# Kernel optimization log

Measured on AMD Instinct MI355X. Metric: run time of the kernel, lower is better.

Reference implementation:

```python
import jax, jax.numpy as jnp
import numpy as np

B, S, D, H, DH = 2, 4096, 768, 12, 64
BS, NB, L, FF, VOCAB = 16, 256, 2, 3072, 50358
SCALE = 1.0 / np.sqrt(DH)


def _ln(x, g, b, eps=1e-12):
    m = jnp.mean(x, -1, keepdims=True)
    v = jnp.var(x, -1, keepdims=True)
    return (x - m) * jax.lax.rsqrt(v + eps) * g + b


def _make_key_block_idx(seed=0):
    rng = np.random.default_rng(seed)
    idx = np.zeros((NB, 7), np.int32)
    allb = np.arange(NB)
    for i in range(NB):
        req = sorted({0, NB - 1, max(i - 1, 0), i, min(i + 1, NB - 1)})
        pool = np.setdiff1d(allb, req)
        extra = rng.choice(pool, size=7 - len(req), replace=False)
        idx[i] = np.concatenate([req, extra])
    return jnp.asarray(idx)


def _sparse_attn(q, k, v, key_idx):
    # q,k,v: [B,H,NB,BS,DH]; key_idx: [NB,7]
    kg = k[:, :, key_idx].reshape(B, H, NB, 7 * BS, DH)  # gather key blocks
    vg = v[:, :, key_idx].reshape(B, H, NB, 7 * BS, DH)
    s = jnp.einsum('bhnqd,bhnkd->bhnqk', q, kg) * SCALE
    o = jnp.einsum('bhnqk,bhnkd->bhnqd', jax.nn.softmax(s, -1), vg)
    # first/last query blocks: full (global) attention over all keys
    qe = q[:, :, jnp.array([0, NB - 1])]                 # [B,H,2,BS,DH]
    kf = k.reshape(B, H, S, DH)
    vf = v.reshape(B, H, S, DH)
    se = jnp.einsum('bhgqd,bhkd->bhgqk', qe, kf) * SCALE
    oe = jnp.einsum('bhgqk,bhkd->bhgqd', jax.nn.softmax(se, -1), vf)
    o = o.at[:, :, 0].set(oe[:, :, 0]).at[:, :, NB - 1].set(oe[:, :, 1])
    # [B,H,NB,BS,DH] -> [B,S,D]
    return o.transpose(0, 2, 3, 1, 4).reshape(B, S, D)


def setup_inputs():
    key = jax.random.key(0)
    ks = iter(jax.random.split(key, 24))
    n = lambda sh, s=0.02: jax.random.normal(next(ks), sh, jnp.float32) * s
    inp = {
        'input_ids': jax.random.randint(next(ks), (B, S), 0, VOCAB),
        'key_block_idx': _make_key_block_idx(),
        'embed': n((VOCAB, D)),
        'Wqkv': n((L, D, 3 * D)), 'bqkv': jnp.zeros((L, 3 * D)),
        'Wo': n((L, D, D)), 'bo': jnp.zeros((L, D)),
        'ln1_g': jnp.ones((L, D)), 'ln1_b': jnp.zeros((L, D)),
        'Wff1': n((L, D, FF)), 'bff1': jnp.zeros((L, FF)),
        'Wff2': n((L, FF, D)), 'bff2': jnp.zeros((L, D)),
        'ln2_g': jnp.ones((L, D)), 'ln2_b': jnp.zeros((L, D)),
        'Wp': n((D, D)), 'bp': jnp.zeros((D,)),
        'start_w': jax.random.normal(next(ks), (D,)),
        'end_w': jax.random.normal(next(ks), (D,)),
        'd1_W': n((D, 20)), 'd1_b': jnp.zeros((20,)),
        'd2_W': n((20, 2)), 'd2_b': jnp.zeros((2,)),
    }
    return inp


def reference(input_ids, key_block_idx, embed, Wqkv, bqkv, Wo, bo, ln1_g, ln1_b,
              Wff1, bff1, Wff2, bff2, ln2_g, ln2_b, Wp, bp, start_w, end_w,
              d1_W, d1_b, d2_W, d2_b):
    x = embed[input_ids]                                  # [B,S,D]
    for l in range(L):
        qkv = x @ Wqkv[l] + bqkv[l]
        q, k, v = jnp.split(qkv, 3, axis=-1)
        blk = lambda t: t.reshape(B, NB, BS, H, DH).transpose(0, 3, 1, 2, 4)
        a = _sparse_attn(blk(q), blk(k), blk(v), key_block_idx)
        x = _ln(x + a @ Wo[l] + bo[l], ln1_g[l], ln1_b[l])
        h = jax.nn.gelu(x @ Wff1[l] + bff1[l]) @ Wff2[l] + bff2[l]
        x = _ln(x + h, ln2_g[l], ln2_b[l])
    pool = jnp.tanh(x[:, 0] @ Wp + bp)                    # BigBird pooler
    start_probs = jax.nn.softmax(x @ start_w, -1)         # [B,S]
    end_probs = jax.nn.softmax(x @ end_w, -1)
    d = (pool[0] @ d1_W + d1_b) @ d2_W + d2_b             # no ReLU, as in source
    disc = jax.nn.softmax(d, -1)
    return start_probs, end_probs, disc
```

## Files before the change

kernel.cpp:

```cpp
#include <hip/hip_runtime.h>
#include <hip/hip_bf16.h>
#include <math.h>

#define B_   2
#define S_   4096
#define D_   768
#define H_   12
#define DH_  64
#define BS_  16
#define NB_  256
#define FF_  3072
#define BT_  (B_ * S_)
#define SCALE_F 0.125f

#define NSPLIT 32
#define TILES_PER_SPLIT (NB_ / NSPLIT)
#define NEDGE (B_ * H_ * 2)
#define NSPARSE (B_ * H_ * NB_)
#define NXCD 8

typedef _Float16 f16x8 __attribute__((ext_vector_type(8)));
typedef _Float16 f16x4 __attribute__((ext_vector_type(4)));
typedef _Float16 f16x2 __attribute__((ext_vector_type(2)));
typedef float    f32x4 __attribute__((ext_vector_type(4)));
typedef float    f32x16 __attribute__((ext_vector_type(16)));

#define DKS 8
#define DKC (D_ / DKS)

#define SV2(v, k) __builtin_shufflevector(v, v, k, (k) + 1)

__device__ __forceinline__ int xcd_swz(int bid, int nwg)
{
    int q = nwg / NXCD;
    return (bid % NXCD) * q + bid / NXCD;
}

__device__ __forceinline__ float dot2acc(f16x2 a, f16x2 b, float c)
{
#if __has_builtin(__builtin_amdgcn_fdot2)
    return __builtin_amdgcn_fdot2(a, b, c, false);
#else
    return c + (float)a[0] * (float)b[0] + (float)a[1] * (float)b[1];
#endif
}

#define GLD16(gp, lp) __builtin_amdgcn_global_load_lds( \
    (const __attribute__((address_space(1))) void*)(gp), \
    (__attribute__((address_space(3))) void*)(lp), 16, 0, 0)

__device__ __forceinline__ float fast_tanh(float z)
{
    float az = fabsf(z);
    float t = __expf(-2.0f * az);
    float r = (1.0f - t) / (1.0f + t);
    return z < 0.f ? -r : r;
}

__device__ __forceinline__ float gelu_tanh(float v)
{
    float v3 = v * v * v;
    return 0.5f * v * (1.0f + fast_tanh(0.79788456080286535588f * (v + 0.044715f * v3)));
}

struct WSeg { const float* src; _Float16* dst; int K; int N; int start; };
struct WSegs { WSeg s[8]; int total; };

__global__ __launch_bounds__(256) void prep_all(
    WSegs segs, const int* __restrict__ ids, const float* __restrict__ emb,
    _Float16* __restrict__ xh)
{
    int bt = blockIdx.x;
    int t = threadIdx.x;
    if (bt < segs.total) {
        __shared__ float tile[32][33];
        int si = 0;
#pragma unroll
        for (int u = 1; u < 8; ++u)
            if (bt >= segs.s[u].start) si = u;
        const WSeg& sg = segs.s[si];
        int tid = bt - sg.start;
        int tn = sg.N >> 5;
        int n0 = (tid % tn) * 32;
        int k0 = (tid / tn) * 32;

        {
            int r = t >> 3, c = (t & 7) * 4;
            f32x4 v = *(const f32x4*)&sg.src[(size_t)(k0 + r) * sg.N + n0 + c];
            tile[r][c + 0] = v[0];
            tile[r][c + 1] = v[1];
            tile[r][c + 2] = v[2];
            tile[r][c + 3] = v[3];
        }
        __syncthreads();
        {
            int r = t >> 3, c = (t & 7) * 4;
            f16x4 o;
            o[0] = (_Float16)tile[c + 0][r];
            o[1] = (_Float16)tile[c + 1][r];
            o[2] = (_Float16)tile[c + 2][r];
            o[3] = (_Float16)tile[c + 3][r];
            *(f16x4*)&sg.dst[(size_t)(n0 + r) * sg.K + k0 + c] = o;
        }
    } else {
        int row = bt - segs.total;
        int id = ids[row];
        const float* src = emb + (size_t)id * D_;
        _Float16* dst16 = xh + (size_t)row * D_;
        for (int d = t; d < D_; d += 256)
            dst16[d] = (_Float16)src[d];
    }
}

template<int MI, int DBUF, int ACT, int OUT16>
__global__ __launch_bounds__(256) void gemm_f16(
    const _Float16* __restrict__ A, const _Float16* __restrict__ Wt,
    const float* __restrict__ bias, void* __restrict__ Cp,
    int M, int N, int K, int NT128)
{
    constexpr int BM = MI * 64;
    constexpr int QA = 2 * MI;
    constexpr int ASZ = BM * 64;
    constexpr int BSZ = 128 * 64;

    __shared__ __attribute__((aligned(16))) _Float16 As[(DBUF ? 2 : 1) * ASZ];
    __shared__ __attribute__((aligned(16))) _Float16 Bs[(DBUF ? 2 : 1) * BSZ];

    int t = threadIdx.x;
    int w = t >> 6, l = t & 63;
    int swz = xcd_swz(blockIdx.x, gridDim.x);
    int bm = (swz / NT128) * BM, bn = (swz % NT128) * 128;
    int wr = (w >> 1) * (MI * 32), wc = (w & 1) * 64;

    f32x16 acc[MI][2];
#pragma unroll
    for (int i = 0; i < MI; ++i)
#pragma unroll
        for (int j = 0; j < 2; ++j)
#pragma unroll
            for (int r = 0; r < 16; ++r) acc[i][j][r] = 0.f;

    const _Float16* gA[QA];
    const _Float16* gB[4];
#pragma unroll
    for (int q = 0; q < QA; ++q) {
        int m = w * QA + q;
        int row = m * 8 + (l >> 3);
        int sc = (l & 7) ^ (row & 7);
        gA[q] = A + (size_t)(bm + row) * K + sc * 8;
    }
#pragma unroll
    for (int q = 0; q < 4; ++q) {
        int m = w * 4 + q;
        int row = m * 8 + (l >> 3);
        int sc = (l & 7) ^ (row & 7);
        gB[q] = Wt + (size_t)(bn + row) * K + sc * 8;
    }

    int aoff[4][MI], boff[4][2];
#pragma unroll
    for (int kk = 0; kk < 4; ++kk) {
        int ch = (kk * 2 + (l >> 5)) ^ (l & 7);
#pragma unroll
        for (int i = 0; i < MI; ++i)
            aoff[kk][i] = (wr + i * 32 + (l & 31)) * 64 + ch * 8;
#pragma unroll
        for (int j = 0; j < 2; ++j)
            boff[kk][j] = (wc + j * 32 + (l & 31)) * 64 + ch * 8;
    }

#define STAGE_(BUF, K0)                                                   \
    {                                                                     \
        _Float16* ab_ = As + (BUF) * ASZ;                                 \
        _Float16* bb_ = Bs + (BUF) * BSZ;                                 \
        _Pragma("unroll")                                                 \
        for (int q = 0; q < QA; ++q)                                      \
            GLD16(gA[q] + (K0), ab_ + (w * QA + q) * 512);                \
        _Pragma("unroll")                                                 \
        for (int q = 0; q < 4; ++q)                                       \
            GLD16(gB[q] + (K0), bb_ + (w * 4 + q) * 512);                 \
    }

#define COMPUTE_(BUF)                                                     \
    {                                                                     \
        const _Float16* ab_ = As + (BUF) * ASZ;                           \
        const _Float16* bb_ = Bs + (BUF) * BSZ;                           \
        _Pragma("unroll")                                                 \
        for (int kk = 0; kk < 4; ++kk) {                                  \
            f16x8 af[MI], bf[2];                                          \
            _Pragma("unroll")                                             \
            for (int i = 0; i < MI; ++i)                                  \
                af[i] = *(const f16x8*)(ab_ + aoff[kk][i]);               \
            _Pragma("unroll")                                             \
            for (int j = 0; j < 2; ++j)                                   \
                bf[j] = *(const f16x8*)(bb_ + boff[kk][j]);               \
            _Pragma("unroll")                                             \
            for (int i = 0; i < MI; ++i)                                  \
                _Pragma("unroll")                                         \
                for (int j = 0; j < 2; ++j)                               \
                    acc[i][j] = __builtin_amdgcn_mfma_f32_32x32x16_f16(   \
                        af[i], bf[j], acc[i][j], 0, 0, 0);                \
        }                                                                 \
    }

    if (DBUF) {
        STAGE_(0, 0);
        __syncthreads();
        int cur = 0;
#pragma unroll 2
        for (int k0 = 0; k0 < K; k0 += 64) {
            if (k0 + 64 < K) STAGE_(cur ^ 1, k0 + 64);
            COMPUTE_(cur);
            __syncthreads();
            cur ^= 1;
        }
    } else {
        for (int k0 = 0; k0 < K; k0 += 64) {
            STAGE_(0, k0);
            __syncthreads();
            COMPUTE_(0);
            __syncthreads();
        }
    }
#undef STAGE_
#undef COMPUTE_

#pragma unroll
    for (int i = 0; i < MI; ++i) {
#pragma unroll
        for (int j = 0; j < 2; ++j) {
            int col = bn + wc + j * 32 + (l & 31);
            float bv = bias[col];
#pragma unroll
            for (int rg = 0; rg < 4; ++rg) {
                int row0 = bm + wr + i * 32 + 8 * rg + 4 * (l >> 5);
#pragma unroll
                for (int r = 0; r < 4; ++r) {
                    float v = acc[i][j][rg * 4 + r] + bv;
                    if (ACT) v = gelu_tanh(v);
                    if (OUT16)
                        ((_Float16*)Cp)[(size_t)(row0 + r) * N + col] = (_Float16)v;
                    else
                        ((float*)Cp)[(size_t)(row0 + r) * N + col] = v;
                }
            }
        }
    }
}

template<int NT, bool EDGE>
__device__ __forceinline__ void attn_block(
    const _Float16* __restrict__ qkv, const int* __restrict__ key_idx,
    _Float16* __restrict__ outp, float* __restrict__ pm,
    float* __restrict__ pl, float* __restrict__ pacc,
    int b, int h, int n, int split, int be,
    _Float16 (*qs)[72], _Float16 (*ks)[16][72],
    _Float16 (*vpl)[8][64][2], _Float16 (*ps16)[24])
{
    int t = threadIdx.x;
    int i = t >> 4;
    int c = t & 15;
    int c4 = c * 4;

    *(f16x4*)&qs[i][c4] =
        *(const f16x4*)&qkv[((size_t)(b * S_ + n * BS_ + i)) * (3 * D_) + h * DH_ + c4];
    int kb0 = EDGE ? split * NT : key_idx[n * 7];
    const _Float16* kp0 = qkv + ((size_t)(b * S_ + kb0 * BS_ + i)) * (3 * D_) + D_ + h * DH_;
    f16x4 kr = *(const f16x4*)(kp0 + c4);
    f16x4 vr = *(const f16x4*)(kp0 + D_ + c4);
    __syncthreads();

    f16x8 qv[8];
#pragma unroll
    for (int d0 = 0; d0 < 8; ++d0) qv[d0] = *(const f16x8*)&qs[i][d0 * 8];

    *(f16x4*)&ks[0][i][c4] = kr;
#pragma unroll
    for (int u = 0; u < 4; ++u) vpl[0][i >> 1][c4 + u][i & 1] = vr[u];
    if (NT > 1) {
        int kb1 = EDGE ? (split * NT + 1) : key_idx[n * 7 + 1];
        const _Float16* kp1 = qkv + ((size_t)(b * S_ + kb1 * BS_ + i)) * (3 * D_) + D_ + h * DH_;
        kr = *(const f16x4*)(kp1 + c4);
        vr = *(const f16x4*)(kp1 + D_ + c4);
    }
    __syncthreads();

    float m_old = -1e30f, lsum = 0.f;
    float acc0 = 0.f, acc1 = 0.f, acc2 = 0.f, acc3 = 0.f;
    const f16x2 one2 = {(_Float16)1.f, (_Float16)1.f};

#pragma unroll 1
    for (int jj = 0; jj < NT; ++jj) {
        int cur = jj & 1;
        if (jj + 1 < NT) {
            *(f16x4*)&ks[cur ^ 1][i][c4] = kr;
#pragma unroll
            for (int u = 0; u < 4; ++u) vpl[cur ^ 1][i >> 1][c4 + u][i & 1] = vr[u];
        }
        if (jj + 2 < NT) {
            int kb2 = EDGE ? (split * NT + jj + 2) : key_idx[n * 7 + jj + 2];
            const _Float16* kp2 = qkv + ((size_t)(b * S_ + kb2 * BS_ + i)) * (3 * D_) + D_ + h * DH_;
            kr = *(const f16x4*)(kp2 + c4);
            vr = *(const f16x4*)(kp2 + D_ + c4);
        }

        __builtin_amdgcn_s_setprio(1);
        float s0 = 0.f, s1 = 0.f;
#pragma unroll
        for (int d0 = 0; d0 < 8; ++d0) {
            f16x8 kv = *(const f16x8*)&ks[cur][c][d0 * 8];
            s0 = dot2acc(SV2(qv[d0], 0), SV2(kv, 0), s0);
            s1 = dot2acc(SV2(qv[d0], 2), SV2(kv, 2), s1);
            s0 = dot2acc(SV2(qv[d0], 4), SV2(kv, 4), s0);
            s1 = dot2acc(SV2(qv[d0], 6), SV2(kv, 6), s1);
        }
        float s = (s0 + s1) * SCALE_F;

        float rm = s;
#pragma unroll
        for (int off = 8; off; off >>= 1) rm = fmaxf(rm, __shfl_xor(rm, off, 64));
        float m_new = fmaxf(m_old, rm);
        float p = __expf(s - m_new);

        ps16[i][c] = (_Float16)p;
        f16x8 plo = *(const f16x8*)&ps16[i][0];
        f16x8 phi = *(const f16x8*)&ps16[i][8];

        float rs = 0.f;
        rs = dot2acc(SV2(plo, 0), one2, rs);
        rs = dot2acc(SV2(plo, 2), one2, rs);
        rs = dot2acc(SV2(plo, 4), one2, rs);
        rs = dot2acc(SV2(plo, 6), one2, rs);
        rs = dot2acc(SV2(phi, 0), one2, rs);
        rs = dot2acc(SV2(phi, 2), one2, rs);
        rs = dot2acc(SV2(phi, 4), one2, rs);
        rs = dot2acc(SV2(phi, 6), one2, rs);

        float corr = __expf(m_old - m_new);
        lsum = lsum * corr + rs;
        acc0 *= corr; acc1 *= corr; acc2 *= corr; acc3 *= corr;

#define PVJ(JP, PSRC, OFF)                                            \
        {                                                             \
            f16x8 vv = *(const f16x8*)&vpl[cur][JP][c4][0];           \
            f16x2 pp = SV2(PSRC, OFF);                                \
            acc0 = dot2acc(pp, SV2(vv, 0), acc0);                     \
            acc1 = dot2acc(pp, SV2(vv, 2), acc1);                     \
            acc2 = dot2acc(pp, SV2(vv, 4), acc2);                     \
            acc3 = dot2acc(pp, SV2(vv, 6), acc3);                     \
        }
        PVJ(0, plo, 0) PVJ(1, plo, 2) PVJ(2, plo, 4) PVJ(3, plo, 6)
        PVJ(4, phi, 0) PVJ(5, phi, 2) PVJ(6, phi, 4) PVJ(7, phi, 6)
#undef PVJ
        __builtin_amdgcn_s_setprio(0);
        m_old = m_new;
        __syncthreads();
    }

    if (EDGE) {
        int psx = (be * NSPLIT + split) * 16 + i;
        if (c == 0) { pm[psx] = m_old; pl[psx] = lsum; }
        float* pd = pacc + (size_t)psx * 64 + c4;
        pd[0] = acc0; pd[1] = acc1; pd[2] = acc2; pd[3] = acc3;
    } else {
        float inv = 1.f / lsum;
        _Float16* dst = outp + ((size_t)(b * S_ + n * BS_ + i)) * D_ + h * DH_ + c4;
        dst[0] = (_Float16)(acc0 * inv);
        dst[1] = (_Float16)(acc1 * inv);
        dst[2] = (_Float16)(acc2 * inv);
        dst[3] = (_Float16)(acc3 * inv);
    }
}

__global__ __launch_bounds__(256) void attn_fused(
    const _Float16* __restrict__ qkv, const int* __restrict__ key_idx,
    _Float16* __restrict__ outp, float* __restrict__ pm,
    float* __restrict__ pl, float* __restrict__ pacc)
{
    __shared__ __attribute__((aligned(16))) _Float16 qs[16][72];
    __shared__ __attribute__((aligned(16))) _Float16 ks[2][16][72];
    __shared__ __attribute__((aligned(16))) _Float16 vpl[2][8][64][2];
    __shared__ __attribute__((aligned(16))) _Float16 ps16[16][24];

    int bi = xcd_swz(blockIdx.x, gridDim.x);
    if (bi < NSPARSE) {
        int n = bi % NB_;
        if (n == 0 || n == NB_ - 1) return;
        int h = (bi / NB_) % H_;
        int b = bi / (NB_ * H_);
        attn_block<7, false>(qkv, key_idx, outp, nullptr, nullptr, nullptr,
                             b, h, n, 0, 0, qs, ks, vpl, ps16);
    } else {
        int ei = bi - NSPARSE;
        int split = ei % NSPLIT;
        int be = ei / NSPLIT;
        int e = be & 1;
        int h = (be >> 1) % H_;
        int b = be / (2 * H_);
        int n = e ? (NB_ - 1) : 0;
        attn_block<TILES_PER_SPLIT, true>(qkv, nullptr, nullptr, pm, pl, pacc,
                                          b, h, n, split, be, qs, ks, vpl, ps16);
    }
}

__global__ __launch_bounds__(256) void attn_edge_combine(
    const float* __restrict__ pm, const float* __restrict__ pl,
    const float* __restrict__ pacc, _Float16* __restrict__ outp)
{
    int be = blockIdx.x;
    int e = be & 1;
    int h = (be >> 1) % H_;
    int b = be / (2 * H_);
    int n = e ? (NB_ - 1) : 0;

    int t = threadIdx.x;
    int i = t >> 4;
    int c = t & 15;

    float M = -1e30f;
#pragma unroll 4
    for (int s = 0; s < NSPLIT; ++s)
        M = fmaxf(M, pm[(be * NSPLIT + s) * 16 + i]);

    float L = 0.f;
    float acc[4] = {0.f, 0.f, 0.f, 0.f};
    for (int s = 0; s < NSPLIT; ++s) {
        int ps = (be * NSPLIT + s) * 16 + i;
        float wgt = __expf(pm[ps] - M);
        L += pl[ps] * wgt;
#pragma unroll
        for (int u = 0; u < 4; ++u) acc[u] += pacc[(size_t)ps * 64 + c * 4 + u] * wgt;
    }

    float inv = 1.f / L;
    _Float16* dst = outp + ((size_t)(b * S_ + n * BS_ + i)) * D_ + h * DH_ + c * 4;
#pragma unroll
    for (int u = 0; u < 4; ++u) dst[u] = (_Float16)(acc[u] * inv);
}

template<int WRITE32>
__global__ __launch_bounds__(256) void add_ln_kernel(
    _Float16* __restrict__ xh, const _Float16* __restrict__ g,
    const float* __restrict__ gamma, const float* __restrict__ beta,
    float* __restrict__ x32)
{
    int row = blockIdx.x;
    int t = threadIdx.x;
    _Float16* xr = xh + (size_t)row * D_;
    const _Float16* gr = g + (size_t)row * D_;

    float v[3];
    float s = 0.f, s2 = 0.f;
#pragma unroll
    for (int r = 0; r < 3; ++r) {
        int d = t + 256 * r;
        v[r] = (float)xr[d] + (float)gr[d];
        s += v[r];
        s2 += v[r] * v[r];
    }
#pragma unroll
    for (int off = 32; off; off >>= 1) {
        s  += __shfl_xor(s, off, 64);
        s2 += __shfl_xor(s2, off, 64);
    }
    __shared__ float sA[4], sB[4];
    int wave = t >> 6, lane = t & 63;
    if (lane == 0) { sA[wave] = s; sB[wave] = s2; }
    __syncthreads();
    s  = sA[0] + sA[1] + sA[2] + sA[3];
    s2 = sB[0] + sB[1] + sB[2] + sB[3];
    float mean = s * (1.0f / D_);
    float var = s2 * (1.0f / D_) - mean * mean;
    float rstd = rsqrtf(var + 1e-12f);
#pragma unroll
    for (int r = 0; r < 3; ++r) {
        int d = t + 256 * r;
        float o = (v[r] - mean) * rstd * gamma[d] + beta[d];
        xr[d] = (_Float16)o;
        if (WRITE32) x32[(size_t)row * D_ + d] = o;
    }
}

__global__ __launch_bounds__(256) void heads_fused(
    const float* __restrict__ x, const float* __restrict__ sw,
    const float* __restrict__ ew, const float* __restrict__ Wp,
    float* __restrict__ sl, float* __restrict__ el,
    float* __restrict__ partial)
{
    int bi = blockIdx.x;
    int t = threadIdx.x;
    if (bi < 2048) {
        int wave = t >> 6, lane = t & 63;
        int row = bi * 4 + wave;
        const float* xr = x + (size_t)row * D_;
        float a = 0.f, e = 0.f;
        for (int d = lane; d < D_; d += 64) {
            float xv = xr[d];
            a += xv * sw[d];
            e += xv * ew[d];
        }
#pragma unroll
        for (int off = 32; off; off >>= 1) {
            a += __shfl_xor(a, off, 64);
            e += __shfl_xor(e, off, 64);
        }
        if (lane == 0) { sl[row] = a; el[row] = e; }
    } else {
        int ei = bi - 2048;
        int jb = ei % 3;
        int ks = ei / 3;
        int j = jb * 256 + t;
        int k0 = ks * DKC;

        __shared__ float xs[DKC];
        if (t < DKC) xs[t] = x[k0 + t];
        __syncthreads();

        float s = 0.f;
#pragma unroll 8
        for (int kk = 0; kk < DKC; ++kk)
            s += xs[kk] * Wp[(size_t)(k0 + kk) * D_ + j];
        partial[ks * D_ + j] = s;
    }
}

__global__ __launch_bounds__(256) void final_fused(
    const float* __restrict__ sl, const float* __restrict__ el,
    const float* __restrict__ partial, const float* __restrict__ bp,
    const float* __restrict__ d1W, const float* __restrict__ d1b,
    const float* __restrict__ d2W, const float* __restrict__ d2b,
    float* __restrict__ outp)
{
    int r = blockIdx.x;
    int t = threadIdx.x;
    if (r < 4) {
        const float* src = (r < 2 ? sl : el) + (size_t)(r & 1) * S_;
        float* dst = outp + (r < 2 ? 0 : BT_) + (size_t)(r & 1) * S_;
        int wave = t >> 6, lane = t & 63;
        __shared__ float sm[4], ss[4];

        float m = -1e30f;
        for (int k = t; k < S_; k += 256) m = fmaxf(m, src[k]);
#pragma unroll
        for (int off = 32; off; off >>= 1) m = fmaxf(m, __shfl_xor(m, off, 64));
        if (lane == 0) sm[wave] = m;
        __syncthreads();
        m = fmaxf(fmaxf(sm[0], sm[1]), fmaxf(sm[2], sm[3]));

        float s = 0.f;
        for (int k = t; k < S_; k += 256) s += __expf(src[k] - m);
#pragma unroll
        for (int off = 32; off; off >>= 1) s += __shfl_xor(s, off, 64);
        if (lane == 0) ss[wave] = s;
        __syncthreads();
        s = ss[0] + ss[1] + ss[2] + ss[3];

        float inv = 1.f / s;
        for (int k = t; k < S_; k += 256) dst[k] = __expf(src[k] - m) * inv;
    } else {
        __shared__ float pool[D_];
        __shared__ float h1[20];
        float* out2 = outp + 2 * BT_;
        for (int j = t; j < D_; j += 256) {
            float s = bp[j];
#pragma unroll
            for (int ks = 0; ks < DKS; ++ks) s += partial[ks * D_ + j];
            pool[j] = tanhf(s);
        }
        __syncthreads();
        if (t < 20) {
            float s = d1b[t];
            for (int k = 0; k < D_; ++k) s += pool[k] * d1W[k * 20 + t];
            h1[t] = s;
        }
        __syncthreads();
        if (t == 0) {
            float d0 = d2b[0], d1v = d2b[1];
#pragma unroll
            for (int u = 0; u < 20; ++u) {
                d0  += h1[u] * d2W[u * 2 + 0];
                d1v += h1[u] * d2W[u * 2 + 1];
            }
            float m = fmaxf(d0, d1v);
            float e0 = __expf(d0 - m), e1 = __expf(d1v - m);
            float inv = 1.f / (e0 + e1);
            out2[0] = e0 * inv;
            out2[1] = e1 * inv;
        }
    }
}

extern "C" void kernel_launch(void* const* d_in, const int* in_sizes, int n_in,
                              void* d_out, int out_size, void* d_ws, size_t ws_size,
                              hipStream_t stream)
{
    const int*   ids   = (const int*)d_in[0];
    const int*   kbi   = (const int*)d_in[1];
    const float* emb   = (const float*)d_in[2];
    const float* Wqkv  = (const float*)d_in[3];
    const float* bqkv  = (const float*)d_in[4];
    const float* Wo    = (const float*)d_in[5];
    const float* bo    = (const float*)d_in[6];
    const float* ln1g  = (const float*)d_in[7];
    const float* ln1b  = (const float*)d_in[8];
    const float* Wff1  = (const float*)d_in[9];
    const float* bff1  = (const float*)d_in[10];
    const float* Wff2  = (const float*)d_in[11];
    const float* bff2  = (const float*)d_in[12];
    const float* ln2g  = (const float*)d_in[13];
    const float* ln2b  = (const float*)d_in[14];
    const float* Wp    = (const float*)d_in[15];
    const float* bp    = (const float*)d_in[16];
    const float* sw    = (const float*)d_in[17];
    const float* ew    = (const float*)d_in[18];
    const float* d1W   = (const float*)d_in[19];
    const float* d1b   = (const float*)d_in[20];
    const float* d2W   = (const float*)d_in[21];
    const float* d2b   = (const float*)d_in[22];
    float* outp = (float*)d_out;

    float* ws   = (float*)d_ws;
    float* x    = ws;
    float* xbf  = x   + (size_t)BT_ * D_;
    float* r1f  = xbf + (size_t)BT_ * D_ / 2;
    float* abf  = r1f + (size_t)BT_ * FF_ / 2;
    float* r2   = abf + (size_t)BT_ * D_ / 2;
    float* wtf  = r2  + (size_t)BT_ * D_;
    float* sl   = wtf + 7077888;
    float* el   = sl  + BT_;
    float* dpar = el  + BT_;

    _Float16* xh    = (_Float16*)xbf;
    _Float16* qkv16 = (_Float16*)r1f;
    _Float16* h16   = (_Float16*)r1f;
    _Float16* ab    = (_Float16*)abf;
    float* pm   = r2;
    float* pl   = r2 + NEDGE * NSPLIT * 16;
    float* pacc = pl + NEDGE * NSPLIT * 16;
    _Float16* g16 = (_Float16*)r2;

    _Float16* Wt    = (_Float16*)wtf;
    _Float16* WqkvT = Wt;
    _Float16* WoT   = WqkvT + (size_t)2 * 2304 * 768;
    _Float16* Wff1T = WoT   + (size_t)2 * 768 * 768;
    _Float16* Wff2T = Wff1T + (size_t)2 * 3072 * 768;

    WSegs segs;
    int start = 0;
    for (int l = 0; l < 2; ++l) {
        int base = l * 4;
        segs.s[base + 0] = { Wqkv + (size_t)l * 768 * 2304,
                             WqkvT + (size_t)l * 2304 * 768, 768, 2304, start };
        start += (2304 / 32) * (768 / 32);
        segs.s[base + 1] = { Wo + (size_t)l * 768 * 768,
                             WoT + (size_t)l * 768 * 768, 768, 768, start };
        start += (768 / 32) * (768 / 32);
        segs.s[base + 2] = { Wff1 + (size_t)l * 768 * 3072,
                             Wff1T + (size_t)l * 3072 * 768, 768, 3072, start };
        start += (3072 / 32) * (768 / 32);
        segs.s[base + 3] = { Wff2 + (size_t)l * 3072 * 768,
                             Wff2T + (size_t)l * 768 * 3072, 3072, 768, start };
        start += (768 / 32) * (3072 / 32);
    }
    segs.total = start;

    prep_all<<<segs.total + BT_, 256, 0, stream>>>(segs, ids, emb, xh);

    for (int l = 0; l < 2; ++l) {
        gemm_f16<2,0,0,1><<<(BT_/128) * (2304/128), 256, 0, stream>>>(
            xh, WqkvT + (size_t)l * 2304 * 768, bqkv + (size_t)l * 3 * D_,
            qkv16, BT_, 3 * D_, D_, 2304/128);
        attn_fused<<<NSPARSE + NEDGE * NSPLIT, 256, 0, stream>>>(
            qkv16, kbi, ab, pm, pl, pacc);
        attn_edge_combine<<<NEDGE, 256, 0, stream>>>(pm, pl, pacc, ab);
        gemm_f16<1,1,0,1><<<(BT_/64) * (768/128), 256, 0, stream>>>(
            ab, WoT + (size_t)l * 768 * 768, bo + (size_t)l * D_,
            g16, BT_, D_, D_, 768/128);
        add_ln_kernel<0><<<BT_, 256, 0, stream>>>(
            xh, g16, ln1g + (size_t)l * D_, ln1b + (size_t)l * D_, nullptr);
        gemm_f16<2,0,1,1><<<(BT_/128) * (3072/128), 256, 0, stream>>>(
            xh, Wff1T + (size_t)l * 3072 * 768, bff1 + (size_t)l * FF_,
            h16, BT_, FF_, D_, 3072/128);
        gemm_f16<1,1,0,1><<<(BT_/64) * (768/128), 256, 0, stream>>>(
            h16, Wff2T + (size_t)l * 768 * 3072, bff2 + (size_t)l * D_,
            g16, BT_, D_, FF_, 768/128);
        if (l == 1)
            add_ln_kernel<1><<<BT_, 256, 0, stream>>>(
                xh, g16, ln2g + (size_t)l * D_, ln2b + (size_t)l * D_, x);
        else
            add_ln_kernel<0><<<BT_, 256, 0, stream>>>(
                xh, g16, ln2g + (size_t)l * D_, ln2b + (size_t)l * D_, nullptr);
    }

    heads_fused<<<2048 + 3 * DKS, 256, 0, stream>>>(x, sw, ew, Wp, sl, el, dpar);
    final_fused<<<5, 256, 0, stream>>>(sl, el, dpar, bp, d1W, d1b, d2W, d2b, outp);
}
```

Measured before the change: 607.6 us.

## Rewrite sparse attention as per-wave MFMA tiles without block barriers

Each 16x16 attention tile is now handled by a single wavefront: QK^T uses two 16x16x32 f16 MFMAs and PV uses four 16x16x16 MFMAs, replacing packed fdot2 loops. Q and K fragments are loaded straight from global memory into registers. Only V goes through a small per-wave LDS buffer to be transposed, which removes the block-wide syncthreads and the double-buffered K/V staging. Four tiles share a 256-thread block, so the grid shrinks by four. The trade-off is that the K/V prefetch pipelining is lost and uncoalesced transposed LDS writes are added.

```diff
diff --git a/kernel.cpp b/kernel.cpp
--- a/kernel.cpp
+++ b/kernel.cpp
@@ -28,21 +28,12 @@
 #define DKS 8
 #define DKC (D_ / DKS)
 
-#define SV2(v, k) __builtin_shufflevector(v, v, k, (k) + 1)
+#define MFMA_PV(a, b, c) __builtin_amdgcn_mfma_f32_16x16x16f16(a, b, c, 0, 0, 0)
 
 __device__ __forceinline__ int xcd_swz(int bid, int nwg)
 {
     int q = nwg / NXCD;
     return (bid % NXCD) * q + bid / NXCD;
-}
-
-__device__ __forceinline__ float dot2acc(f16x2 a, f16x2 b, float c)
-{
-#if __has_builtin(__builtin_amdgcn_fdot2)
-    return __builtin_amdgcn_fdot2(a, b, c, false);
-#else
-    return c + (float)a[0] * (float)b[0] + (float)a[1] * (float)b[1];
-#endif
 }
 
 #define GLD16(gp, lp) __builtin_amdgcn_global_load_lds( \
@@ -249,126 +240,104 @@
 }
 
 template<int NT, bool EDGE>
-__device__ __forceinline__ void attn_block(
+__device__ __forceinline__ void attn_wave(
     const _Float16* __restrict__ qkv, const int* __restrict__ key_idx,
     _Float16* __restrict__ outp, float* __restrict__ pm,
     float* __restrict__ pl, float* __restrict__ pacc,
     int b, int h, int n, int split, int be,
-    _Float16 (*qs)[72], _Float16 (*ks)[16][72],
-    _Float16 (*vpl)[8][64][2], _Float16 (*ps16)[24])
-{
-    int t = threadIdx.x;
-    int i = t >> 4;
-    int c = t & 15;
-    int c4 = c * 4;
-
-    *(f16x4*)&qs[i][c4] =
-        *(const f16x4*)&qkv[((size_t)(b * S_ + n * BS_ + i)) * (3 * D_) + h * DH_ + c4];
-    int kb0 = EDGE ? split * NT : key_idx[n * 7];
-    const _Float16* kp0 = qkv + ((size_t)(b * S_ + kb0 * BS_ + i)) * (3 * D_) + D_ + h * DH_;
-    f16x4 kr = *(const f16x4*)(kp0 + c4);
-    f16x4 vr = *(const f16x4*)(kp0 + D_ + c4);
-    __syncthreads();
-
-    f16x8 qv[8];
-#pragma unroll
-    for (int d0 = 0; d0 < 8; ++d0) qv[d0] = *(const f16x8*)&qs[i][d0 * 8];
-
-    *(f16x4*)&ks[0][i][c4] = kr;
-#pragma unroll
-    for (int u = 0; u < 4; ++u) vpl[0][i >> 1][c4 + u][i & 1] = vr[u];
-    if (NT > 1) {
-        int kb1 = EDGE ? (split * NT + 1) : key_idx[n * 7 + 1];
-        const _Float16* kp1 = qkv + ((size_t)(b * S_ + kb1 * BS_ + i)) * (3 * D_) + D_ + h * DH_;
-        kr = *(const f16x4*)(kp1 + c4);
-        vr = *(const f16x4*)(kp1 + D_ + c4);
-    }
-    __syncthreads();
+    _Float16 (*vq)[24])
+{
+    int l = threadIdx.x & 63;
+    int q = l & 15;
+    int g = l >> 4;
+
+    const _Float16* qp = qkv + ((size_t)(b * S_ + n * BS_ + q)) * (3 * D_) + h * DH_ + g * 8;
+    f16x8 qf0 = *(const f16x8*)qp;
+    f16x8 qf1 = *(const f16x8*)(qp + 32);
 
     float m_old = -1e30f, lsum = 0.f;
-    float acc0 = 0.f, acc1 = 0.f, acc2 = 0.f, acc3 = 0.f;
-    const f16x2 one2 = {(_Float16)1.f, (_Float16)1.f};
+    f32x4 o[4];
+#pragma unroll
+    for (int db = 0; db < 4; ++db) o[db] = (f32x4){0.f, 0.f, 0.f, 0.f};
 
 #pragma unroll 1
     for (int jj = 0; jj < NT; ++jj) {
-        int cur = jj & 1;
-        if (jj + 1 < NT) {
-            *(f16x4*)&ks[cur ^ 1][i][c4] = kr;
-#pragma unroll
-            for (int u = 0; u < 4; ++u) vpl[cur ^ 1][i >> 1][c4 + u][i & 1] = vr[u];
-        }
-        if (jj + 2 < NT) {
-            int kb2 = EDGE ? (split * NT + jj + 2) : key_idx[n * 7 + jj + 2];
-            const _Float16* kp2 = qkv + ((size_t)(b * S_ + kb2 * BS_ + i)) * (3 * D_) + D_ + h * DH_;
-            kr = *(const f16x4*)(kp2 + c4);
-            vr = *(const f16x4*)(kp2 + D_ + c4);
-        }
-
-        __builtin_amdgcn_s_setprio(1);
-        float s0 = 0.f, s1 = 0.f;
-#pragma unroll
-        for (int d0 = 0; d0 < 8; ++d0) {
-            f16x8 kv = *(const f16x8*)&ks[cur][c][d0 * 8];
-            s0 = dot2acc(SV2(qv[d0], 0), SV2(kv, 0), s0);
-            s1 = dot2acc(SV2(qv[d0], 2), SV2(kv, 2), s1);
-            s0 = dot2acc(SV2(qv[d0], 4), SV2(kv, 4), s0);
-            s1 = dot2acc(SV2(qv[d0], 6), SV2(kv, 6), s1);
-        }
-        float s = (s0 + s1) * SCALE_F;
-
-        float rm = s;
-#pragma unroll
-        for (int off = 8; off; off >>= 1) rm = fmaxf(rm, __shfl_xor(rm, off, 64));
-        float m_new = fmaxf(m_old, rm);
-        float p = __expf(s - m_new);
-
-        ps16[i][c] = (_Float16)p;
-        f16x8 plo = *(const f16x8*)&ps16[i][0];
-        f16x8 phi = *(const f16x8*)&ps16[i][8];
-
+        int kb = EDGE ? (split * NT + jj) : key_idx[n * 7 + jj];
+        const _Float16* kvrow = qkv + ((size_t)(b * S_ + kb * BS_ + q)) * (3 * D_);
+
+        f16x8 kf0 = *(const f16x8*)(kvrow + D_ + h * DH_ + g * 8);
+        f16x8 kf1 = *(const f16x8*)(kvrow + D_ + h * DH_ + g * 8 + 32);
+
+        {
+            const _Float16* vp = kvrow + 2 * D_ + h * DH_ + g * 16;
+            f16x8 v0 = *(const f16x8*)vp;
+            f16x8 v1 = *(const f16x8*)(vp + 8);
+#pragma unroll
+            for (int u = 0; u < 8; ++u) vq[g * 16 + u][q] = v0[u];
+#pragma unroll
+            for (int u = 0; u < 8; ++u) vq[g * 16 + 8 + u][q] = v1[u];
+        }
+
+        f32x4 sc = (f32x4){0.f, 0.f, 0.f, 0.f};
+        sc = __builtin_amdgcn_mfma_f32_16x16x32_f16(kf0, qf0, sc, 0, 0, 0);
+        sc = __builtin_amdgcn_mfma_f32_16x16x32_f16(kf1, qf1, sc, 0, 0, 0);
+#pragma unroll
+        for (int r = 0; r < 4; ++r) sc[r] *= SCALE_F;
+
+        float tm = fmaxf(fmaxf(sc[0], sc[1]), fmaxf(sc[2], sc[3]));
+        tm = fmaxf(tm, __shfl_xor(tm, 16, 64));
+        tm = fmaxf(tm, __shfl_xor(tm, 32, 64));
+        float m_new = fmaxf(m_old, tm);
+
+        float pr[4];
         float rs = 0.f;
-        rs = dot2acc(SV2(plo, 0), one2, rs);
-        rs = dot2acc(SV2(plo, 2), one2, rs);
-        rs = dot2acc(SV2(plo, 4), one2, rs);
-        rs = dot2acc(SV2(plo, 6), one2, rs);
-        rs = dot2acc(SV2(phi, 0), one2, rs);
-        rs = dot2acc(SV2(phi, 2), one2, rs);
-        rs = dot2acc(SV2(phi, 4), one2, rs);
-        rs = dot2acc(SV2(phi, 6), one2, rs);
+#pragma unroll
+        for (int r = 0; r < 4; ++r) { pr[r] = __expf(sc[r] - m_new); rs += pr[r]; }
+        rs += __shfl_xor(rs, 16, 64);
+        rs += __shfl_xor(rs, 32, 64);
 
         float corr = __expf(m_old - m_new);
         lsum = lsum * corr + rs;
-        acc0 *= corr; acc1 *= corr; acc2 *= corr; acc3 *= corr;
-
-#define PVJ(JP, PSRC, OFF)                                            \
-        {                                                             \
-            f16x8 vv = *(const f16x8*)&vpl[cur][JP][c4][0];           \
-            f16x2 pp = SV2(PSRC, OFF);                                \
-            acc0 = dot2acc(pp, SV2(vv, 0), acc0);                     \
-            acc1 = dot2acc(pp, SV2(vv, 2), acc1);                     \
-            acc2 = dot2acc(pp, SV2(vv, 4), acc2);                     \
-            acc3 = dot2acc(pp, SV2(vv, 6), acc3);                     \
-        }
-        PVJ(0, plo, 0) PVJ(1, plo, 2) PVJ(2, plo, 4) PVJ(3, plo, 6)
-        PVJ(4, phi, 0) PVJ(5, phi, 2) PVJ(6, phi, 4) PVJ(7, phi, 6)
-#undef PVJ
-        __builtin_amdgcn_s_setprio(0);
         m_old = m_new;
-        __syncthreads();
+
+        float cq[4];
+#pragma unroll
+        for (int r = 0; r < 4; ++r) cq[r] = __shfl(corr, g * 4 + r, 64);
+#pragma unroll
+        for (int db = 0; db < 4; ++db)
+#pragma unroll
+            for (int r = 0; r < 4; ++r) o[db][r] *= cq[r];
+
+        f16x4 pa;
+#pragma unroll
+        for (int r = 0; r < 4; ++r) pa[r] = (_Float16)pr[r];
+
+#pragma unroll
+        for (int db = 0; db < 4; ++db) {
+            f16x4 vb = *(const f16x4*)&vq[db * 16 + q][g * 4];
+            o[db] = MFMA_PV(pa, vb, o[db]);
+        }
     }
 
     if (EDGE) {
-        int psx = (be * NSPLIT + split) * 16 + i;
-        if (c == 0) { pm[psx] = m_old; pl[psx] = lsum; }
-        float* pd = pacc + (size_t)psx * 64 + c4;
-        pd[0] = acc0; pd[1] = acc1; pd[2] = acc2; pd[3] = acc3;
+        int base16 = (be * NSPLIT + split) * 16;
+        if (l < 16) { pm[base16 + l] = m_old; pl[base16 + l] = lsum; }
+#pragma unroll
+        for (int db = 0; db < 4; ++db)
+#pragma unroll
+            for (int r = 0; r < 4; ++r)
+                pacc[(size_t)(base16 + g * 4 + r) * 64 + db * 16 + q] = o[db][r];
     } else {
-        float inv = 1.f / lsum;
-        _Float16* dst = outp + ((size_t)(b * S_ + n * BS_ + i)) * D_ + h * DH_ + c4;
-        dst[0] = (_Float16)(acc0 * inv);
-        dst[1] = (_Float16)(acc1 * inv);
-        dst[2] = (_Float16)(acc2 * inv);
-        dst[3] = (_Float16)(acc3 * inv);
+        float linv[4];
+#pragma unroll
+        for (int r = 0; r < 4; ++r) linv[r] = 1.f / __shfl(lsum, g * 4 + r, 64);
+#pragma unroll
+        for (int r = 0; r < 4; ++r) {
+            _Float16* dst = outp + ((size_t)(b * S_ + n * BS_ + g * 4 + r)) * D_ + h * DH_ + q;
+#pragma unroll
+            for (int db = 0; db < 4; ++db)
+                dst[db * 16] = (_Float16)(o[db][r] * linv[r]);
+        }
     }
 }
 
@@ -377,19 +346,18 @@
     _Float16* __restrict__ outp, float* __restrict__ pm,
     float* __restrict__ pl, float* __restrict__ pacc)
 {
-    __shared__ __attribute__((aligned(16))) _Float16 qs[16][72];
-    __shared__ __attribute__((aligned(16))) _Float16 ks[2][16][72];
-    __shared__ __attribute__((aligned(16))) _Float16 vpl[2][8][64][2];
-    __shared__ __attribute__((aligned(16))) _Float16 ps16[16][24];
-
-    int bi = xcd_swz(blockIdx.x, gridDim.x);
+    __shared__ __attribute__((aligned(16))) _Float16 vqs[4][64][24];
+
+    int w = threadIdx.x >> 6;
+    int bi = xcd_swz(blockIdx.x, gridDim.x) * 4 + w;
+
     if (bi < NSPARSE) {
         int n = bi % NB_;
         if (n == 0 || n == NB_ - 1) return;
         int h = (bi / NB_) % H_;
         int b = bi / (NB_ * H_);
-        attn_block<7, false>(qkv, key_idx, outp, nullptr, nullptr, nullptr,
-                             b, h, n, 0, 0, qs, ks, vpl, ps16);
+        attn_wave<7, false>(qkv, key_idx, outp, nullptr, nullptr, nullptr,
+                            b, h, n, 0, 0, vqs[w]);
     } else {
         int ei = bi - NSPARSE;
         int split = ei % NSPLIT;
@@ -398,8 +366,8 @@
         int h = (be >> 1) % H_;
         int b = be / (2 * H_);
         int n = e ? (NB_ - 1) : 0;
-        attn_block<TILES_PER_SPLIT, true>(qkv, nullptr, nullptr, pm, pl, pacc,
-                                          b, h, n, split, be, qs, ks, vpl, ps16);
+        attn_wave<TILES_PER_SPLIT, true>(qkv, nullptr, nullptr, pm, pl, pacc,
+                                         b, h, n, split, be, vqs[w]);
     }
 }
 
@@ -670,7 +638,7 @@
         gemm_f16<2,0,0,1><<<(BT_/128) * (2304/128), 256, 0, stream>>>(
             xh, WqkvT + (size_t)l * 2304 * 768, bqkv + (size_t)l * 3 * D_,
             qkv16, BT_, 3 * D_, D_, 2304/128);
-        attn_fused<<<NSPARSE + NEDGE * NSPLIT, 256, 0, stream>>>(
+        attn_fused<<<(NSPARSE + NEDGE * NSPLIT) / 4, 256, 0, stream>>>(
             qkv16, kbi, ab, pm, pl, pacc);
         attn_edge_combine<<<NEDGE, 256, 0, stream>>>(pm, pl, pacc, ab);
         gemm_f16<1,1,0,1><<<(BT_/64) * (768/128), 256, 0, stream>>>(
```

Measured after the change: 549.6 us, median of 2. -9.5%, faster.
